# Kernel optimization log

Hardware: AMD Instinct MI355X
Metric: run time of the kernel (lower is better)

Reference implementation:

```python
import jax, jax.numpy as jnp
import numpy as np


def setup_inputs() -> dict:
    key = jax.random.key(0)
    k1, k2, k3, k4 = jax.random.split(key, 4)
    B, Nq, Nk, D = 8, 2048, 2048, 768
    return {
        "query": jax.random.normal(k1, (B, Nq, D), dtype=jnp.float32),
        "key": jax.random.normal(k2, (Nk, D), dtype=jnp.float32),
        "x": jax.random.normal(k3, (B, Nk, D), dtype=jnp.float32),
        "W": jax.random.normal(k4, (D, D), dtype=jnp.float32) * (1.0 / np.sqrt(D)),
        "b": jnp.zeros((D,), dtype=jnp.float32),
    }


def reference(query, key, x, W, b):
    # Linear projection: [B,Nq,dk] @ W^T + b -> [B,Nq,dq]
    query_proj = jnp.einsum("bqd,ed->bqe", query, W) + b
    # tensordot over dim_query: [B,Nq,dq] x [Nk,dq] -> [B,Nq,Nk]
    score = jnp.einsum("bqe,ke->bqk", query_proj, key)
    attn = jax.nn.softmax(score, axis=-1)
    # bmm: [B,Nq,Nk] @ [B,Nk,Dv] -> [B,Nq,Dv]
    out = jnp.einsum("bqk,bkd->bqd", attn, x)
    return (out, attn)
```

## Files before the change

kernel.cpp:

```cpp
#include <hip/hip_runtime.h>

typedef short s16x8 __attribute__((ext_vector_type(8)));
typedef _Float16 h16x8 __attribute__((ext_vector_type(8)));
typedef float f32x4 __attribute__((ext_vector_type(4)));

__device__ __forceinline__ unsigned short f2bf(float f) {
    unsigned int u = __builtin_bit_cast(unsigned int, f);
    u += 0x7FFFu + ((u >> 16) & 1u);
    return (unsigned short)(u >> 16);
}
__device__ __forceinline__ float bf2f(unsigned short h) {
    unsigned int u = ((unsigned int)h) << 16;
    return __builtin_bit_cast(float, u);
}
__device__ __forceinline__ unsigned short f2h(float f) {
    _Float16 h = (_Float16)f;
    return __builtin_bit_cast(unsigned short, h);
}
__device__ __forceinline__ float h2f(unsigned short u) {
    return (float)__builtin_bit_cast(_Float16, u);
}

__device__ __forceinline__ int swz(int row, int kbyte) {
    return (row * 64 + kbyte) ^ (((row >> 1) & 3) << 4);
}

__device__ __forceinline__ void gl16(const void* g, void* l) {
    __builtin_amdgcn_global_load_lds(
        (__attribute__((address_space(1))) void*)(g),
        (__attribute__((address_space(3))) void*)(l), 16, 0, 0);
}

#define STG(ptr, rowbase, tau, bufp, slot) do {                                     \
    gl16((ptr) + (long)((rowbase) + sl) * K + (tau) * 64 + koff,                    \
         &lds[bufp][slot][(unsigned)t * 8]);                                        \
    gl16((ptr) + (long)((rowbase) + 64 + sl) * K + (tau) * 64 + koff,               \
         &lds[bufp][slot][4096u + (unsigned)t * 8]);                                \
} while (0)

#define PH(bufp, qi, qj, VMSTR, STAGEBLOCK) do {                                    \
    h16x8 af_[2][4], bf_[2][2];                                                     \
    const char* baseA_ = (const char*)&lds[bufp][qi][0];                            \
    const char* baseB_ = (const char*)&lds[bufp][2 + (qj)][0];                      \
    _Pragma("unroll")                                                               \
    for (int ks_ = 0; ks_ < 2; ++ks_) {                                             \
        _Pragma("unroll")                                                           \
        for (int f_ = 0; f_ < 4; ++f_) {                                            \
            const int row_ = wm * 64 + f_ * 16 + lr;                                \
            af_[ks_][f_] = *(const h16x8*)(baseA_ + row_ * 128 +                    \
                            ((ks_ * 64 + kg16) ^ ((row_ & 7) << 4)));               \
        }                                                                           \
        _Pragma("unroll")                                                           \
        for (int g_ = 0; g_ < 2; ++g_) {                                            \
            const int row_ = wn * 32 + g_ * 16 + lr;                                \
            bf_[ks_][g_] = *(const h16x8*)(baseB_ + row_ * 128 +                    \
                            ((ks_ * 64 + kg16) ^ ((row_ & 7) << 4)));               \
        }                                                                           \
    }                                                                               \
    STAGEBLOCK;                                                                     \
    asm volatile("s_waitcnt vmcnt(" VMSTR ")" ::: "memory");                        \
    __builtin_amdgcn_s_barrier();                                                   \
    __builtin_amdgcn_sched_barrier(0);                                              \
    __builtin_amdgcn_s_setprio(1);                                                  \
    _Pragma("unroll")                                                               \
    for (int ks_ = 0; ks_ < 2; ++ks_)                                               \
        _Pragma("unroll")                                                           \
        for (int f_ = 0; f_ < 4; ++f_)                                              \
            _Pragma("unroll")                                                       \
            for (int g_ = 0; g_ < 2; ++g_)                                          \
                acc[qi][qj][f_][g_] = __builtin_amdgcn_mfma_f32_16x16x32_f16(       \
                    af_[ks_][f_], bf_[ks_][g_], acc[qi][qj][f_][g_], 0, 0, 0);      \
    __builtin_amdgcn_s_setprio(0);                                                  \
    __builtin_amdgcn_s_barrier();                                                   \
    __builtin_amdgcn_sched_barrier(0);                                              \
} while (0)

__global__ __launch_bounds__(512, 2) void score_8ph(
    const unsigned short* __restrict__ A, const unsigned short* __restrict__ Bm,
    const float* __restrict__ bias, float* __restrict__ C,
    int M, int N, int K, int nbx)
{
    __shared__ unsigned short lds[2][4][8192];

    const int bid = blockIdx.x;
    const int cpx = gridDim.x >> 3;
    const int sw  = (bid & 7) * cpx + (bid >> 3);
    const int m0 = (sw / nbx) * 256, n0 = (sw % nbx) * 256;

    const int t = threadIdx.x;
    const int l = t & 63, w = t >> 6;
    const int wm = w >> 2, wn = w & 3;
    const int lr = l & 15;
    const int kg16 = (l >> 4) * 16;

    const int sl   = w * 8 + (l >> 3);
    const int koff = ((l & 7) ^ (sl & 7)) * 8;

    f32x4 acc[2][2][4][2];
    #pragma unroll
    for (int a = 0; a < 2; ++a)
        #pragma unroll
        for (int b = 0; b < 2; ++b)
            #pragma unroll
            for (int c = 0; c < 4; ++c)
                #pragma unroll
                for (int d = 0; d < 2; ++d)
                    acc[a][b][c][d] = (f32x4){0.f, 0.f, 0.f, 0.f};

    const int nt = K >> 6;

    STG(A,  m0,       0, 0, 0);
    STG(Bm, n0,       0, 0, 2);
    STG(A,  m0 + 128, 0, 0, 1);
    STG(Bm, n0 + 128, 0, 0, 3);
    STG(A,  m0,       1, 1, 0);
    STG(Bm, n0,       1, 1, 2);
    asm volatile("s_waitcnt vmcnt(8)" ::: "memory");
    __builtin_amdgcn_s_barrier();
    __builtin_amdgcn_sched_barrier(0);

    int tau = 0;
    for (; tau < nt - 2; ++tau) {
        const int bp = tau & 1;
        PH(bp, 0, 0, "6",  { STG(A,  m0 + 128, tau + 1, bp ^ 1, 1); });
        PH(bp, 0, 1, "10", { STG(Bm, n0 + 128, tau + 1, bp ^ 1, 3); });
        PH(bp, 1, 0, "10", { STG(A,  m0,       tau + 2, bp,     0); });
        PH(bp, 1, 1, "8",  { STG(Bm, n0,       tau + 2, bp,     2); });
    }
    {
        const int bp = tau & 1;
        PH(bp, 0, 0, "6",  { STG(A,  m0 + 128, tau + 1, bp ^ 1, 1); });
        PH(bp, 0, 1, "10", { STG(Bm, n0 + 128, tau + 1, bp ^ 1, 3); });
        PH(bp, 1, 0, "10", {});
        PH(bp, 1, 1, "8",  {});
        ++tau;
    }
    {
        const int bp = tau & 1;
        PH(bp, 0, 0, "0", {});
        PH(bp, 0, 1, "0", {});
        PH(bp, 1, 0, "0", {});
        PH(bp, 1, 1, "0", {});
    }

    #pragma unroll
    for (int qi = 0; qi < 2; ++qi)
        #pragma unroll
        for (int qj = 0; qj < 2; ++qj)
            #pragma unroll
            for (int f = 0; f < 4; ++f)
                #pragma unroll
                for (int g = 0; g < 2; ++g) {
                    const int row = m0 + qi * 128 + wm * 64 + f * 16 + (l >> 4) * 4;
                    const int col = n0 + qj * 128 + wn * 32 + g * 16 + lr;
                    const float badd = bias[col];
                    #pragma unroll
                    for (int r = 0; r < 4; ++r)
                        C[(long)(row + r) * N + col] = acc[qi][qj][f][g][r] + badd;
                }
}

__global__ __launch_bounds__(256, 1) void pv_2ph(
    const unsigned short* __restrict__ A, const unsigned short* __restrict__ Bm,
    float* __restrict__ C, int M, int N, int K,
    long strideA, long strideB, long strideC)
{
    __shared__ unsigned short lds[2][2][128 * 64];

    const int bz = blockIdx.z;
    const unsigned short* Ab = A  + (long)bz * strideA;
    const unsigned short* Bb = Bm + (long)bz * strideB;
    float* Cb = C + (long)bz * strideC;
    const int m0 = blockIdx.x * 128, n0 = blockIdx.y * 128;

    const int t = threadIdx.x;
    const int l = t & 63, w = t >> 6;
    const int rm = (w >> 1) * 64, cn = (w & 1) * 64;
    const int lr = l & 15;
    const int kg16 = (l >> 4) * 16;

    const int jrow   = l >> 3;
    const int srcoff = ((l & 7) ^ jrow) << 3;

    const unsigned short* gA = Ab + (long)(m0 + jrow) * K + srcoff;
    const unsigned short* gB = Bb + (long)(n0 + jrow) * K + srcoff;

    f32x4 acc[4][4];
    #pragma unroll
    for (int i = 0; i < 4; ++i)
        #pragma unroll
        for (int j = 0; j < 4; ++j)
            acc[i][j] = (f32x4){0.f, 0.f, 0.f, 0.f};

    const int nt = K >> 6;
    #pragma unroll
    for (int i = 0; i < 4; ++i) {
        const int c = w * 4 + i;
        gl16(gA + (long)(8 * c) * K, &lds[0][0][c * 512]);
        gl16(gB + (long)(8 * c) * K, &lds[0][1][c * 512]);
    }
    __syncthreads();

    int p = 0;
    for (int it = 0; it < nt; ++it) {
        if (it + 1 < nt) {
            const unsigned short* nA = gA + (it + 1) * 64;
            const unsigned short* nB = gB + (it + 1) * 64;
            #pragma unroll
            for (int i = 0; i < 4; ++i) {
                const int c = w * 4 + i;
                gl16(nA + (long)(8 * c) * K, &lds[p ^ 1][0][c * 512]);
                gl16(nB + (long)(8 * c) * K, &lds[p ^ 1][1][c * 512]);
            }
        }
        const char* baseA = (const char*)&lds[p][0][0];
        const char* baseB = (const char*)&lds[p][1][0];
        h16x8 af[2][4], bf[2][4];
        #pragma unroll
        for (int ks = 0; ks < 2; ++ks)
            #pragma unroll
            for (int mi = 0; mi < 4; ++mi) {
                const int row = rm + mi * 16 + lr;
                af[ks][mi] = *(const h16x8*)(baseA + row * 128 +
                                ((ks * 64 + kg16) ^ ((row & 7) << 4)));
            }
        #pragma unroll
        for (int ks = 0; ks < 2; ++ks)
            #pragma unroll
            for (int nj = 0; nj < 4; ++nj) {
                const int row = cn + nj * 16 + lr;
                bf[ks][nj] = *(const h16x8*)(baseB + row * 128 +
                                ((ks * 64 + kg16) ^ ((row & 7) << 4)));
            }
        #pragma unroll
        for (int ks = 0; ks < 2; ++ks)
            #pragma unroll
            for (int mi = 0; mi < 4; ++mi)
                #pragma unroll
                for (int nj = 0; nj < 4; ++nj)
                    acc[mi][nj] = __builtin_amdgcn_mfma_f32_16x16x32_f16(
                        af[ks][mi], bf[ks][nj], acc[mi][nj], 0, 0, 0);
        __syncthreads();
        p ^= 1;
    }

    #pragma unroll
    for (int mi = 0; mi < 4; ++mi) {
        #pragma unroll
        for (int nj = 0; nj < 4; ++nj) {
            const int row = m0 + rm + mi * 16 + (l >> 4) * 4;
            const int col = n0 + cn + nj * 16 + lr;
            #pragma unroll
            for (int r = 0; r < 4; ++r)
                Cb[(long)(row + r) * N + col] = acc[mi][nj][r];
        }
    }
}

template<int SPLIT, bool TRANSB, bool BIAS>
__global__ __launch_bounds__(256, 1) void mfma_gemm(
    const float* __restrict__ A, const float* __restrict__ Bsrc,
    const float* __restrict__ bias, float* __restrict__ C,
    int M, int N, int K, long strideA, long strideB, long strideC)
{
    constexpr int NB = (SPLIT > 1) ? 2 : 1;
    __shared__ unsigned short sA[NB][128 * 32];
    __shared__ unsigned short sB[NB][128 * 32];

    const int t  = threadIdx.x;
    const int bz = blockIdx.z;
    const float* Ab = A    + (long)bz * strideA;
    const float* Bb = Bsrc + (long)bz * strideB;
    float*       Cb = C    + (long)bz * strideC;
    const int m0 = blockIdx.y * 128;
    const int n0 = blockIdx.x * 128;

    const int l  = t & 63, w = t >> 6;
    const int rm = (w >> 1) * 64;
    const int cn = (w & 1) * 64;
    const int lr = l & 15;
    const int kg = (l >> 4) * 16;

    const int srow = t >> 1;
    const int skh  = (t & 1) * 16;
    const int s_ = t & 15;
    const int kp = t >> 4;

    f32x4 acc[4][4];
    #pragma unroll
    for (int i = 0; i < 4; ++i)
        #pragma unroll
        for (int j = 0; j < 4; ++j)
            acc[i][j] = (f32x4){0.f, 0.f, 0.f, 0.f};

    for (int kt = 0; kt < K; kt += 32) {
        {
            const float* p = &Ab[(long)(m0 + srow) * K + kt + skh];
            float f[16];
            #pragma unroll
            for (int q = 0; q < 4; ++q) {
                const float4 v = *(const float4*)(p + 4 * q);
                f[4*q+0] = v.x; f[4*q+1] = v.y; f[4*q+2] = v.z; f[4*q+3] = v.w;
            }
            s16x8 h0, h1, l0, l1;
            #pragma unroll
            for (int q = 0; q < 8; ++q) {
                unsigned short h = f2bf(f[q]);      h0[q] = (short)h;
                if (SPLIT > 1) l0[q] = (short)f2bf(f[q] - bf2f(h));
                unsigned short g = f2bf(f[8 + q]);  h1[q] = (short)g;
                if (SPLIT > 1) l1[q] = (short)f2bf(f[8 + q] - bf2f(g));
            }
            *(s16x8*)((char*)sA[0] + swz(srow, skh * 2))      = h0;
            *(s16x8*)((char*)sA[0] + swz(srow, skh * 2 + 16)) = h1;
            if (SPLIT > 1) {
                *(s16x8*)((char*)sA[1] + swz(srow, skh * 2))      = l0;
                *(s16x8*)((char*)sA[1] + swz(srow, skh * 2 + 16)) = l1;
            }
        }
        if (!TRANSB) {
            const float* p = &Bb[(long)(n0 + srow) * K + kt + skh];
            float f[16];
            #pragma unroll
            for (int q = 0; q < 4; ++q) {
                const float4 v = *(const float4*)(p + 4 * q);
                f[4*q+0] = v.x; f[4*q+1] = v.y; f[4*q+2] = v.z; f[4*q+3] = v.w;
            }
            s16x8 h0, h1, l0, l1;
            #pragma unroll
            for (int q = 0; q < 8; ++q) {
                unsigned short h = f2bf(f[q]);      h0[q] = (short)h;
                if (SPLIT > 1) l0[q] = (short)f2bf(f[q] - bf2f(h));
                unsigned short g = f2bf(f[8 + q]);  h1[q] = (short)g;
                if (SPLIT > 1) l1[q] = (short)f2bf(f[8 + q] - bf2f(g));
            }
            *(s16x8*)((char*)sB[0] + swz(srow, skh * 2))      = h0;
            *(s16x8*)((char*)sB[0] + swz(srow, skh * 2 + 16)) = h1;
            if (SPLIT > 1) {
                *(s16x8*)((char*)sB[1] + swz(srow, skh * 2))      = l0;
                *(s16x8*)((char*)sB[1] + swz(srow, skh * 2 + 16)) = l1;
            }
        } else {
            const float* r0 = &Bb[(long)(kt + 2 * kp) * N + n0 + s_ * 8];
            const float* r1 = r0 + N;
            float a0[8], a1[8];
            {
                const float4 u0 = *(const float4*)(r0);
                const float4 u1 = *(const float4*)(r0 + 4);
                const float4 v0 = *(const float4*)(r1);
                const float4 v1 = *(const float4*)(r1 + 4);
                a0[0]=u0.x;a0[1]=u0.y;a0[2]=u0.z;a0[3]=u0.w;
                a0[4]=u1.x;a0[5]=u1.y;a0[6]=u1.z;a0[7]=u1.w;
                a1[0]=v0.x;a1[1]=v0.y;a1[2]=v0.z;a1[3]=v0.w;
                a1[4]=v1.x;a1[5]=v1.y;a1[6]=v1.z;a1[7]=v1.w;
            }
            #pragma unroll
            for (int j = 0; j < 8; ++j) {
                const int i  = (j + s_) & 7;
                const int nl = s_ * 8 + i;
                const unsigned int val =
                    (unsigned int)f2bf(a0[i]) | ((unsigned int)f2bf(a1[i]) << 16);
                *(unsigned int*)((char*)sB[0] + swz(nl, 4 * kp)) = val;
            }
        }
        __syncthreads();

        s16x8 ah[4], bh[4];
        #pragma unroll
        for (int mi = 0; mi < 4; ++mi)
            ah[mi] = *(const s16x8*)((const char*)sA[0] + swz(rm + mi * 16 + lr, kg));
        #pragma unroll
        for (int nj = 0; nj < 4; ++nj)
            bh[nj] = *(const s16x8*)((const char*)sB[0] + swz(cn + nj * 16 + lr, kg));
        #pragma unroll
        for (int mi = 0; mi < 4; ++mi)
            #pragma unroll
            for (int nj = 0; nj < 4; ++nj)
                acc[mi][nj] = __builtin_amdgcn_mfma_f32_16x16x32_bf16(
                    ah[mi], bh[nj], acc[mi][nj], 0, 0, 0);
        if (SPLIT > 1) {
            s16x8 al[4], bl[4];
            #pragma unroll
            for (int mi = 0; mi < 4; ++mi)
                al[mi] = *(const s16x8*)((const char*)sA[1] + swz(rm + mi * 16 + lr, kg));
            #pragma unroll
            for (int mi = 0; mi < 4; ++mi)
                #pragma unroll
                for (int nj = 0; nj < 4; ++nj)
                    acc[mi][nj] = __builtin_amdgcn_mfma_f32_16x16x32_bf16(
                        al[mi], bh[nj], acc[mi][nj], 0, 0, 0);
            #pragma unroll
            for (int nj = 0; nj < 4; ++nj)
                bl[nj] = *(const s16x8*)((const char*)sB[1] + swz(cn + nj * 16 + lr, kg));
            #pragma unroll
            for (int mi = 0; mi < 4; ++mi)
                #pragma unroll
                for (int nj = 0; nj < 4; ++nj)
                    acc[mi][nj] = __builtin_amdgcn_mfma_f32_16x16x32_bf16(
                        ah[mi], bl[nj], acc[mi][nj], 0, 0, 0);
        }
        __syncthreads();
    }

    #pragma unroll
    for (int mi = 0; mi < 4; ++mi) {
        #pragma unroll
        for (int nj = 0; nj < 4; ++nj) {
            const int row = m0 + rm + mi * 16 + (l >> 4) * 4;
            const int col = n0 + cn + nj * 16 + lr;
            const float badd = BIAS ? bias[col] : 0.f;
            #pragma unroll
            for (int r = 0; r < 4; ++r)
                Cb[(long)(row + r) * N + col] = acc[mi][nj][r] + badd;
        }
    }
}

__global__ __launch_bounds__(256, 1) void score_gemm(
    const unsigned short* __restrict__ Ah, const unsigned short* __restrict__ Al,
    const unsigned short* __restrict__ Bh, const unsigned short* __restrict__ Bl,
    const float* __restrict__ bias, float* __restrict__ C,
    int M, int N, int K, int nbx)
{
    __shared__ unsigned short sAh[128 * 32];
    __shared__ unsigned short sBh[128 * 32];
    __shared__ unsigned short sAl[128 * 32];
    __shared__ unsigned short sBl[128 * 32];

    const int bid = blockIdx.x;
    const int cpx = gridDim.x >> 3;
    const int sw  = (bid & 7) * cpx + (bid >> 3);
    const int mb  = sw / nbx, nb = sw % nbx;
    const int m0 = mb * 128, n0 = nb * 128;

    const int t = threadIdx.x;
    const int l = t & 63, w = t >> 6;
    const int rm = (w >> 1) * 64;
    const int cn = (w & 1) * 64;
    const int lr = l & 15;
    const int kg = (l >> 4) * 16;

    const int r0 = 2 * w, r1 = 2 * w + 1;
    const int rowS0 = 16 * r0 + (l >> 2);
    const int rowS1 = 16 * r1 + (l >> 2);
    const int h0 = (l & 3) ^ ((rowS0 >> 1) & 3);
    const int h1 = (l & 3) ^ ((rowS1 >> 1) & 3);

    const unsigned short* gAh0 = Ah + (long)(m0 + rowS0) * K + 8 * h0;
    const unsigned short* gAh1 = Ah + (long)(m0 + rowS1) * K + 8 * h1;
    const unsigned short* gAl0 = Al + (long)(m0 + rowS0) * K + 8 * h0;
    const unsigned short* gAl1 = Al + (long)(m0 + rowS1) * K + 8 * h1;
    const unsigned short* gBh0 = Bh + (long)(n0 + rowS0) * K + 8 * h0;
    const unsigned short* gBh1 = Bh + (long)(n0 + rowS1) * K + 8 * h1;
    const unsigned short* gBl0 = Bl + (long)(n0 + rowS0) * K + 8 * h0;
    const unsigned short* gBl1 = Bl + (long)(n0 + rowS1) * K + 8 * h1;

    unsigned short* dA0 = &sAh[r0 * 512];
    unsigned short* dA1 = &sAh[r1 * 512];
    unsigned short* dAl0 = &sAl[r0 * 512];
    unsigned short* dAl1 = &sAl[r1 * 512];
    unsigned short* dB0 = &sBh[r0 * 512];
    unsigned short* dB1 = &sBh[r1 * 512];
    unsigned short* dBl0 = &sBl[r0 * 512];
    unsigned short* dBl1 = &sBl[r1 * 512];

    f32x4 acc[4][4];
    #pragma unroll
    for (int i = 0; i < 4; ++i)
        #pragma unroll
        for (int j = 0; j < 4; ++j)
            acc[i][j] = (f32x4){0.f, 0.f, 0.f, 0.f};

    const int nk = K >> 5;
    for (int it = 0; it < nk; ++it) {
        gl16(gAh0, dA0);  gl16(gAh1, dA1);
        gl16(gBh0, dB0);  gl16(gBh1, dB1);
        gl16(gAl0, dAl0); gl16(gAl1, dAl1);
        gl16(gBl0, dBl0); gl16(gBl1, dBl1);
        gAh0 += 32; gAh1 += 32; gAl0 += 32; gAl1 += 32;
        gBh0 += 32; gBh1 += 32; gBl0 += 32; gBl1 += 32;
        __syncthreads();

        s16x8 ah[4], bh[4];
        #pragma unroll
        for (int mi = 0; mi < 4; ++mi)
            ah[mi] = *(const s16x8*)((const char*)sAh + swz(rm + mi * 16 + lr, kg));
        #pragma unroll
        for (int nj = 0; nj < 4; ++nj)
            bh[nj] = *(const s16x8*)((const char*)sBh + swz(cn + nj * 16 + lr, kg));
        #pragma unroll
        for (int mi = 0; mi < 4; ++mi)
            #pragma unroll
            for (int nj = 0; nj < 4; ++nj)
                acc[mi][nj] = __builtin_amdgcn_mfma_f32_16x16x32_bf16(
                    ah[mi], bh[nj], acc[mi][nj], 0, 0, 0);
        s16x8 al[4], bl[4];
        #pragma unroll
        for (int mi = 0; mi < 4; ++mi)
            al[mi] = *(const s16x8*)((const char*)sAl + swz(rm + mi * 16 + lr, kg));
        #pragma unroll
        for (int mi = 0; mi < 4; ++mi)
            #pragma unroll
            for (int nj = 0; nj < 4; ++nj)
                acc[mi][nj] = __builtin_amdgcn_mfma_f32_16x16x32_bf16(
                    al[mi], bh[nj], acc[mi][nj], 0, 0, 0);
        #pragma unroll
        for (int nj = 0; nj < 4; ++nj)
            bl[nj] = *(const s16x8*)((const char*)sBl + swz(cn + nj * 16 + lr, kg));
        #pragma unroll
        for (int mi = 0; mi < 4; ++mi)
            #pragma unroll
            for (int nj = 0; nj < 4; ++nj)
                acc[mi][nj] = __builtin_amdgcn_mfma_f32_16x16x32_bf16(
                    ah[mi], bl[nj], acc[mi][nj], 0, 0, 0);
        __syncthreads();
    }

    #pragma unroll
    for (int mi = 0; mi < 4; ++mi) {
        #pragma unroll
        for (int nj = 0; nj < 4; ++nj) {
            const int row = m0 + rm + mi * 16 + (l >> 4) * 4;
            const int col = n0 + cn + nj * 16 + lr;
            const float badd = bias[col];
            #pragma unroll
            for (int r = 0; r < 4; ++r)
                C[(long)(row + r) * N + col] = acc[mi][nj][r] + badd;
        }
    }
}

__global__ __launch_bounds__(256, 1) void out_gemm(
    const float* __restrict__ A32, const unsigned short* __restrict__ B16,
    float* __restrict__ C, int M, int N, int K,
    long strideA, long strideB, long strideC)
{
    __shared__ unsigned short sA[128 * 32];
    __shared__ unsigned short sB[128 * 32];

    const int bz = blockIdx.z;
    const float* Ab = A32 + (long)bz * strideA;
    const unsigned short* Bb = B16 + (long)bz * strideB;
    float* Cb = C + (long)bz * strideC;
    const int m0 = blockIdx.x * 128;
    const int n0 = blockIdx.y * 128;

    const int t = threadIdx.x;
    const int l = t & 63, w = t >> 6;
    const int rm = (w >> 1) * 64;
    const int cn = (w & 1) * 64;
    const int lr = l & 15;
    const int kg = (l >> 4) * 16;

    const int r0 = 2 * w, r1 = 2 * w + 1;
    const int rowS0 = 16 * r0 + (l >> 2);
    const int rowS1 = 16 * r1 + (l >> 2);
    const int h0 = (l & 3) ^ ((rowS0 >> 1) & 3);
    const int h1 = (l & 3) ^ ((rowS1 >> 1) & 3);
    const unsigned short* gB0 = Bb + (long)(n0 + rowS0) * K + 8 * h0;
    const unsigned short* gB1 = Bb + (long)(n0 + rowS1) * K + 8 * h1;
    unsigned short* dB0 = &sB[r0 * 512];
    unsigned short* dB1 = &sB[r1 * 512];

    const int srow = t >> 1;
    const int skh  = (t & 1) * 16;
    const float* gA = &Ab[(long)(m0 + srow) * K + skh];

    f32x4 acc[4][4];
    #pragma unroll
    for (int i = 0; i < 4; ++i)
        #pragma unroll
        for (int j = 0; j < 4; ++j)
            acc[i][j] = (f32x4){0.f, 0.f, 0.f, 0.f};

    const int nk = K >> 5;
    for (int it = 0; it < nk; ++it) {
        gl16(gB0, dB0); gl16(gB1, dB1);
        gB0 += 32; gB1 += 32;
        {
            float f[16];
            #pragma unroll
            for (int q = 0; q < 4; ++q) {
                const float4 v = *(const float4*)(gA + 4 * q);
                f[4*q+0] = v.x; f[4*q+1] = v.y; f[4*q+2] = v.z; f[4*q+3] = v.w;
            }
            gA += 32;
            s16x8 v0, v1;
            #pragma unroll
            for (int q = 0; q < 8; ++q) {
                v0[q] = (short)f2bf(f[q]);
                v1[q] = (short)f2bf(f[8 + q]);
            }
            *(s16x8*)((char*)sA + swz(srow, skh * 2))      = v0;
            *(s16x8*)((char*)sA + swz(srow, skh * 2 + 16)) = v1;
        }
        __syncthreads();

        s16x8 ah[4], bh[4];
        #pragma unroll
        for (int mi = 0; mi < 4; ++mi)
            ah[mi] = *(const s16x8*)((const char*)sA + swz(rm + mi * 16 + lr, kg));
        #pragma unroll
        for (int nj = 0; nj < 4; ++nj)
            bh[nj] = *(const s16x8*)((const char*)sB + swz(cn + nj * 16 + lr, kg));
        #pragma unroll
        for (int mi = 0; mi < 4; ++mi)
            #pragma unroll
            for (int nj = 0; nj < 4; ++nj)
                acc[mi][nj] = __builtin_amdgcn_mfma_f32_16x16x32_bf16(
                    ah[mi], bh[nj], acc[mi][nj], 0, 0, 0);
        __syncthreads();
    }

    #pragma unroll
    for (int mi = 0; mi < 4; ++mi) {
        #pragma unroll
        for (int nj = 0; nj < 4; ++nj) {
            const int row = m0 + rm + mi * 16 + (l >> 4) * 4;
            const int col = n0 + cn + nj * 16 + lr;
            #pragma unroll
            for (int r = 0; r < 4; ++r)
                Cb[(long)(row + r) * N + col] = acc[mi][nj][r];
        }
    }
}

template<int MODE>
__global__ __launch_bounds__(256) void transpose64(
    const float* __restrict__ in, void* __restrict__ outv,
    int R, int Cc, long sIn, long sOut)
{
    __shared__ float tl[64][65];
    const int z = blockIdx.z;
    const float* ib = in + (long)z * sIn;
    const int r0 = blockIdx.x * 64, c0 = blockIdx.y * 64;
    const int t = threadIdx.x;
    const int lrr = t >> 4, lc = (t & 15) * 4;
    #pragma unroll
    for (int p = 0; p < 4; ++p) {
        const float4 v = *(const float4*)&ib[(long)(r0 + lrr + 16 * p) * Cc + c0 + lc];
        tl[lrr + 16 * p][lc + 0] = v.x; tl[lrr + 16 * p][lc + 1] = v.y;
        tl[lrr + 16 * p][lc + 2] = v.z; tl[lrr + 16 * p][lc + 3] = v.w;
    }
    __syncthreads();
    #pragma unroll
    for (int p = 0; p < 4; ++p) {
        const int orow = c0 + lrr + 16 * p;
        const int ocol = r0 + lc;
        const float a = tl[lc + 0][lrr + 16 * p];
        const float b = tl[lc + 1][lrr + 16 * p];
        const float c = tl[lc + 2][lrr + 16 * p];
        const float d = tl[lc + 3][lrr + 16 * p];
        if (MODE == 1) {
            ushort4 u = { f2bf(a), f2bf(b), f2bf(c), f2bf(d) };
            *(ushort4*)((unsigned short*)outv + (long)z * sOut + (long)orow * R + ocol) = u;
        } else if (MODE == 2) {
            ushort4 u = { f2h(a), f2h(b), f2h(c), f2h(d) };
            *(ushort4*)((unsigned short*)outv + (long)z * sOut + (long)orow * R + ocol) = u;
        } else {
            float4 u = { a, b, c, d };
            *(float4*)((float*)outv + (long)z * sOut + (long)orow * R + ocol) = u;
        }
    }
}

__global__ __launch_bounds__(256) void convert_hilo(
    const float* __restrict__ src, unsigned short* __restrict__ hi,
    unsigned short* __restrict__ lo, long n8)
{
    for (long i = (long)blockIdx.x * blockDim.x + threadIdx.x; i < n8;
         i += (long)gridDim.x * blockDim.x) {
        const float4 a = *(const float4*)&src[i * 8];
        const float4 b = *(const float4*)&src[i * 8 + 4];
        const float f[8] = { a.x, a.y, a.z, a.w, b.x, b.y, b.z, b.w };
        s16x8 h, lv;
        #pragma unroll
        for (int q = 0; q < 8; ++q) {
            const unsigned short hh = f2bf(f[q]);
            h[q]  = (short)hh;
            lv[q] = (short)f2bf(f[q] - bf2f(hh));
        }
        *(s16x8*)&hi[i * 8] = h;
        *(s16x8*)&lo[i * 8] = lv;
    }
}

__global__ __launch_bounds__(256) void convert_q_ilv(
    const float* __restrict__ src, unsigned short* __restrict__ dst,
    int kd8, long n8)
{
    const int Kd = kd8 * 8;
    for (long i = (long)blockIdx.x * blockDim.x + threadIdx.x; i < n8;
         i += (long)gridDim.x * blockDim.x) {
        const long row = i / kd8;
        const int  col = (int)(i - row * kd8) * 8;
        const float4 a = *(const float4*)&src[i * 8];
        const float4 b = *(const float4*)&src[i * 8 + 4];
        const float f[8] = { a.x, a.y, a.z, a.w, b.x, b.y, b.z, b.w };
        s16x8 h, lv;
        #pragma unroll
        for (int q = 0; q < 8; ++q) {
            const unsigned short hh = f2h(f[q]);
            h[q]  = (short)hh;
            lv[q] = (short)f2h(f[q] - h2f(hh));
        }
        unsigned short* dr = dst + row * (long)(2 * Kd);
        *(s16x8*)&dr[col]      = h;
        *(s16x8*)&dr[Kd + col] = lv;
    }
}

__global__ __launch_bounds__(256) void convert_kw_dup(
    const float* __restrict__ src, unsigned short* __restrict__ dst,
    int kd8, long n8)
{
    const int Kd = kd8 * 8;
    for (long i = (long)blockIdx.x * blockDim.x + threadIdx.x; i < n8;
         i += (long)gridDim.x * blockDim.x) {
        const long row = i / kd8;
        const int  col = (int)(i - row * kd8) * 8;
        const float4 a = *(const float4*)&src[i * 8];
        const float4 b = *(const float4*)&src[i * 8 + 4];
        const float f[8] = { a.x, a.y, a.z, a.w, b.x, b.y, b.z, b.w };
        s16x8 h;
        #pragma unroll
        for (int q = 0; q < 8; ++q) h[q] = (short)f2h(f[q]);
        unsigned short* dr = dst + row * (long)(2 * Kd);
        *(s16x8*)&dr[col]      = h;
        *(s16x8*)&dr[Kd + col] = h;
    }
}

__global__ __launch_bounds__(256) void bk_dot(
    const float* __restrict__ key, const float* __restrict__ b,
    float* __restrict__ bk, int D)
{
    const int row = blockIdx.x * 4 + (threadIdx.x >> 6);
    const int l = threadIdx.x & 63;
    const float* kr = key + (long)row * D;
    float s = 0.f;
    for (int e = l; e < D; e += 64) s += kr[e] * b[e];
    #pragma unroll
    for (int off = 32; off > 0; off >>= 1) s += __shfl_xor(s, off);
    if (l == 0) bk[row] = s;
}

__global__ __launch_bounds__(256) void softmax_f16(
    float* __restrict__ S, unsigned short* __restrict__ S16, int cols)
{
    const long row = blockIdx.x;
    float* p = S + row * (long)cols;
    unsigned short* p16 = S16 + row * (long)cols;
    const int t = threadIdx.x;
    const int wid = t >> 6;
    const int base = t * 8;

    const float4 a = *(const float4*)&p[base];
    const float4 b = *(const float4*)&p[base + 4];
    float vals[8] = { a.x, a.y, a.z, a.w, b.x, b.y, b.z, b.w };
    float m = -INFINITY;
    #pragma unroll
    for (int i = 0; i < 8; ++i) m = fmaxf(m, vals[i]);
    #pragma unroll
    for (int off = 32; off > 0; off >>= 1)
        m = fmaxf(m, __shfl_xor(m, off));
    __shared__ float smax[4], ssum[4];
    if ((t & 63) == 0) smax[wid] = m;
    __syncthreads();
    m = fmaxf(fmaxf(smax[0], smax[1]), fmaxf(smax[2], smax[3]));

    float s = 0.f;
    #pragma unroll
    for (int i = 0; i < 8; ++i) {
        vals[i] = __expf(vals[i] - m);
        s += vals[i];
    }
    #pragma unroll
    for (int off = 32; off > 0; off >>= 1)
        s += __shfl_xor(s, off);
    if ((t & 63) == 0) ssum[wid] = s;
    __syncthreads();
    s = (ssum[0] + ssum[1]) + (ssum[2] + ssum[3]);
    const float inv = 1.0f / s;

    float4 o0, o1;
    o0.x = vals[0]*inv; o0.y = vals[1]*inv; o0.z = vals[2]*inv; o0.w = vals[3]*inv;
    o1.x = vals[4]*inv; o1.y = vals[5]*inv; o1.z = vals[6]*inv; o1.w = vals[7]*inv;
    *(float4*)&p[base]     = o0;
    *(float4*)&p[base + 4] = o1;
    s16x8 h;
    h[0]=(short)f2h(o0.x); h[1]=(short)f2h(o0.y); h[2]=(short)f2h(o0.z); h[3]=(short)f2h(o0.w);
    h[4]=(short)f2h(o1.x); h[5]=(short)f2h(o1.y); h[6]=(short)f2h(o1.z); h[7]=(short)f2h(o1.w);
    *(s16x8*)&p16[base] = h;
}

__global__ __launch_bounds__(256) void softmax_rows(float* __restrict__ S, int cols)
{
    const long row = blockIdx.x;
    float* p = S + row * (long)cols;
    const int t = threadIdx.x;
    const int wid = t >> 6;

    float vals[8];
    float m = -INFINITY;
    #pragma unroll
    for (int i = 0; i < 8; ++i) {
        vals[i] = p[t + i * 256];
        m = fmaxf(m, vals[i]);
    }
    #pragma unroll
    for (int off = 32; off > 0; off >>= 1)
        m = fmaxf(m, __shfl_xor(m, off));
    __shared__ float smax[4], ssum[4];
    if ((t & 63) == 0) smax[wid] = m;
    __syncthreads();
    m = fmaxf(fmaxf(smax[0], smax[1]), fmaxf(smax[2], smax[3]));

    float s = 0.f;
    #pragma unroll
    for (int i = 0; i < 8; ++i) {
        vals[i] = __expf(vals[i] - m);
        s += vals[i];
    }
    #pragma unroll
    for (int off = 32; off > 0; off >>= 1)
        s += __shfl_xor(s, off);
    if ((t & 63) == 0) ssum[wid] = s;
    __syncthreads();
    s = (ssum[0] + ssum[1]) + (ssum[2] + ssum[3]);
    const float inv = 1.0f / s;
    #pragma unroll
    for (int i = 0; i < 8; ++i)
        p[t + i * 256] = vals[i] * inv;
}

extern "C" void kernel_launch(void* const* d_in, const int* in_sizes, int n_in,
                              void* d_out, int out_size, void* d_ws, size_t ws_size,
                              hipStream_t stream)
{
    const float* query = (const float*)d_in[0];
    const float* key   = (const float*)d_in[1];
    const float* x     = (const float*)d_in[2];
    const float* W     = (const float*)d_in[3];
    const float* bias  = (const float*)d_in[4];

    const int D  = in_sizes[4];
    const int Nk = in_sizes[1] / D;
    const int B  = in_sizes[2] / (Nk * D);
    const int Nq = in_sizes[0] / (B * D);

    float* out  = (float*)d_out;
    float* attn = out + (long)B * Nq * D;

    const long nQ  = (long)B * Nq * D;
    const long nKW = (long)Nk * D;
    const long nX  = (long)B * Nk * D;
    const int  M   = B * Nq;
    const int  K2  = 2 * D;

    const size_t xTb    = (size_t)nX * 2;
    const size_t kwDupB = (size_t)Nk * K2 * 2;
    const size_t bkB    = (size_t)Nk * 4;
    const size_t atb1   = (size_t)Nq * Nk * 2;
    const size_t fixedB = xTb + kwDupB + bkB;
    const size_t qLob   = (size_t)nQ * 2;
    const size_t wsMid  = xTb + qLob;

    int g = 0;
    if (ws_size >= fixedB + 2 * atb1) {
        g = (int)((ws_size - fixedB) / atb1);
        if (g > B) g = B;
    }

    if (g >= 2) {
        unsigned short* qIlv  = (unsigned short*)out;
        unsigned short* xT     = (unsigned short*)d_ws;
        unsigned short* kwDup  = (unsigned short*)((char*)d_ws + xTb);
        float*          bk     = (float*)((char*)d_ws + xTb + kwDupB);
        unsigned short* attn16 = (unsigned short*)((char*)d_ws + fixedB);
        float* Wt  = attn;
        float* KWf = attn + 1048576;

        dim3 gtw(D / 64, D / 64, 1);
        transpose64<0><<<gtw, 256, 0, stream>>>(W, Wt, D, D, 0L, 0L);
        dim3 gkw(D / 128, Nk / 128, 1);
        mfma_gemm<3, false, false><<<gkw, 256, 0, stream>>>(
            key, Wt, nullptr, KWf, Nk, D, D, 0L, 0L, 0L);
        convert_kw_dup<<<768, 256, 0, stream>>>(KWf, kwDup, D / 8, nKW / 8);
        bk_dot<<<Nk / 4, 256, 0, stream>>>(key, bias, bk, D);
        convert_q_ilv<<<2048, 256, 0, stream>>>(query, qIlv, D / 8, nQ / 8);
        dim3 gtx(Nk / 64, D / 64, B);
        transpose64<2><<<gtx, 256, 0, stream>>>(
            x, xT, Nk, D, (long)Nk * D, (long)D * Nk);

        const int nbx = Nk / 256;
        const int nwg = (M / 256) * nbx;
        score_8ph<<<nwg, 512, 0, stream>>>(
            qIlv, kwDup, bk, attn, M, Nk, K2, nbx);

        for (int b0 = 0; b0 < B; b0 += g) {
            const int gb = (b0 + g <= B) ? g : (B - b0);
            softmax_f16<<<gb * Nq, 256, 0, stream>>>(
                attn + (long)b0 * Nq * Nk, attn16, Nk);
            dim3 go(Nq / 128, D / 128, gb);
            pv_2ph<<<go, 256, 0, stream>>>(
                attn16, xT + (long)b0 * D * Nk, out + (long)b0 * Nq * D,
                Nq, D, Nk, (long)Nq * Nk, (long)D * Nk, (long)Nq * D);
        }
    } else if (ws_size >= wsMid) {
        unsigned short* q_hi  = (unsigned short*)out;
        unsigned short* KW_hi = q_hi + nQ;
        unsigned short* KW_lo = KW_hi + nKW;
        float*          bk    = (float*)(KW_lo + nKW);
        unsigned short* q_lo  = (unsigned short*)d_ws;
        unsigned short* xT    = q_lo + nQ;
        float* Wt  = attn;
        float* KWf = attn + 1048576;

        dim3 gtw(D / 64, D / 64, 1);
        transpose64<0><<<gtw, 256, 0, stream>>>(W, Wt, D, D, 0L, 0L);
        dim3 gkw(D / 128, Nk / 128, 1);
        mfma_gemm<3, false, false><<<gkw, 256, 0, stream>>>(
            key, Wt, nullptr, KWf, Nk, D, D, 0L, 0L, 0L);
        convert_hilo<<<768, 256, 0, stream>>>(KWf, KW_hi, KW_lo, nKW / 8);
        bk_dot<<<Nk / 4, 256, 0, stream>>>(key, bias, bk, D);
        convert_hilo<<<2048, 256, 0, stream>>>(query, q_hi, q_lo, nQ / 8);
        dim3 gtx(Nk / 64, D / 64, B);
        transpose64<1><<<gtx, 256, 0, stream>>>(
            x, xT, Nk, D, (long)Nk * D, (long)D * Nk);
        const int nbx = Nk / 128;
        const int nwg = (B * Nq / 128) * nbx;
        score_gemm<<<nwg, 256, 0, stream>>>(
            q_hi, q_lo, KW_hi, KW_lo, bk, attn, B * Nq, Nk, D, nbx);
        softmax_rows<<<B * Nq, 256, 0, stream>>>(attn, Nk);
        dim3 go(Nq / 128, D / 128, B);
        out_gemm<<<go, 256, 0, stream>>>(
            attn, xT, out, Nq, D, Nk, (long)Nq * Nk, (long)D * Nk, (long)Nq * D);
    } else {
        float* qp = out;
        dim3 g1(D / 128, (B * Nq) / 128, 1);
        mfma_gemm<3, false, true><<<g1, 256, 0, stream>>>(
            query, W, bias, qp, B * Nq, D, D, 0L, 0L, 0L);
        dim3 g2(Nk / 128, Nq / 128, B);
        mfma_gemm<3, false, false><<<g2, 256, 0, stream>>>(
            qp, key, nullptr, attn, Nq, Nk, D, (long)Nq * D, 0L, (long)Nq * Nk);
        softmax_rows<<<B * Nq, 256, 0, stream>>>(attn, Nk);
        dim3 g4(D / 128, Nq / 128, B);
        mfma_gemm<1, true, false><<<g4, 256, 0, stream>>>(
            attn, x, nullptr, out, Nq, D, Nk, (long)Nq * Nk, (long)Nk * D, (long)Nq * D);
    }
}
```

Measured before the change: 348.8 us.

## Reuse LDS fragments across quadrant phases with serpentine MFMA ordering

Restructures the 8-wave score GEMM main loop so A and B fragments read from LDS are kept in registers and reused across quadrant phases. The new order is (0,0),(0,1),(1,1),(1,0), and staging order and vmcnt thresholds are reworked to match. This cuts LDS reads per K-tile from four A+B fragment sets to two A and two B. In exchange it holds more fragment registers live, which may pressure occupancy at the 512x2 launch bound, and the changed wait counts must stay correct.

```diff
diff --git a/kernel.cpp b/kernel.cpp
--- a/kernel.cpp
+++ b/kernel.cpp
@@ -31,36 +31,44 @@
         (__attribute__((address_space(3))) void*)(l), 16, 0, 0);
 }
 
-#define STG(ptr, rowbase, tau, bufp, slot) do {                                     \
-    gl16((ptr) + (long)((rowbase) + sl) * K + (tau) * 64 + koff,                    \
+#define STG(ptr, rowbase, tt, bufp, slot) do {                                      \
+    gl16((ptr) + (long)((rowbase) + sl) * K + (tt) * 64 + koff,                     \
          &lds[bufp][slot][(unsigned)t * 8]);                                        \
-    gl16((ptr) + (long)((rowbase) + 64 + sl) * K + (tau) * 64 + koff,               \
+    gl16((ptr) + (long)((rowbase) + 64 + sl) * K + (tt) * 64 + koff,                \
          &lds[bufp][slot][4096u + (unsigned)t * 8]);                                \
 } while (0)
 
-#define PH(bufp, qi, qj, VMSTR, STAGEBLOCK) do {                                    \
-    h16x8 af_[2][4], bf_[2][2];                                                     \
-    const char* baseA_ = (const char*)&lds[bufp][qi][0];                            \
-    const char* baseB_ = (const char*)&lds[bufp][2 + (qj)][0];                      \
+#define LDA(qi_) do {                                                               \
+    const char* ba_ = (const char*)&lds[bp][qi_][0];                                \
     _Pragma("unroll")                                                               \
-    for (int ks_ = 0; ks_ < 2; ++ks_) {                                             \
+    for (int ks_ = 0; ks_ < 2; ++ks_)                                               \
         _Pragma("unroll")                                                           \
         for (int f_ = 0; f_ < 4; ++f_) {                                            \
             const int row_ = wm * 64 + f_ * 16 + lr;                                \
-            af_[ks_][f_] = *(const h16x8*)(baseA_ + row_ * 128 +                    \
+            af[ks_][f_] = *(const h16x8*)(ba_ + row_ * 128 +                        \
                             ((ks_ * 64 + kg16) ^ ((row_ & 7) << 4)));               \
         }                                                                           \
+} while (0)
+
+#define LDB(dst_, qj_) do {                                                         \
+    const char* bb_ = (const char*)&lds[bp][2 + (qj_)][0];                          \
+    _Pragma("unroll")                                                               \
+    for (int ks_ = 0; ks_ < 2; ++ks_)                                               \
         _Pragma("unroll")                                                           \
         for (int g_ = 0; g_ < 2; ++g_) {                                            \
             const int row_ = wn * 32 + g_ * 16 + lr;                                \
-            bf_[ks_][g_] = *(const h16x8*)(baseB_ + row_ * 128 +                    \
+            dst_[ks_][g_] = *(const h16x8*)(bb_ + row_ * 128 +                      \
                             ((ks_ * 64 + kg16) ^ ((row_ & 7) << 4)));               \
         }                                                                           \
-    }                                                                               \
-    STAGEBLOCK;                                                                     \
+} while (0)
+
+#define SYNCV(VMSTR) do {                                                           \
     asm volatile("s_waitcnt vmcnt(" VMSTR ")" ::: "memory");                        \
     __builtin_amdgcn_s_barrier();                                                   \
     __builtin_amdgcn_sched_barrier(0);                                              \
+} while (0)
+
+#define MM(qi_, qj_, bfv_) do {                                                     \
     __builtin_amdgcn_s_setprio(1);                                                  \
     _Pragma("unroll")                                                               \
     for (int ks_ = 0; ks_ < 2; ++ks_)                                               \
@@ -68,8 +76,8 @@
         for (int f_ = 0; f_ < 4; ++f_)                                              \
             _Pragma("unroll")                                                       \
             for (int g_ = 0; g_ < 2; ++g_)                                          \
-                acc[qi][qj][f_][g_] = __builtin_amdgcn_mfma_f32_16x16x32_f16(       \
-                    af_[ks_][f_], bf_[ks_][g_], acc[qi][qj][f_][g_], 0, 0, 0);      \
+                acc[qi_][qj_][f_][g_] = __builtin_amdgcn_mfma_f32_16x16x32_f16(     \
+                    af[ks_][f_], bfv_[ks_][g_], acc[qi_][qj_][f_][g_], 0, 0, 0);    \
     __builtin_amdgcn_s_setprio(0);                                                  \
     __builtin_amdgcn_s_barrier();                                                   \
     __builtin_amdgcn_sched_barrier(0);                                              \
@@ -96,6 +104,7 @@
     const int sl   = w * 8 + (l >> 3);
     const int koff = ((l & 7) ^ (sl & 7)) * 8;
 
+    h16x8 af[2][4], bf0[2][2], bf1[2][2];
     f32x4 acc[2][2][4][2];
     #pragma unroll
     for (int a = 0; a < 2; ++a)
@@ -111,8 +120,8 @@
 
     STG(A,  m0,       0, 0, 0);
     STG(Bm, n0,       0, 0, 2);
+    STG(Bm, n0 + 128, 0, 0, 3);
     STG(A,  m0 + 128, 0, 0, 1);
-    STG(Bm, n0 + 128, 0, 0, 3);
     STG(A,  m0,       1, 1, 0);
     STG(Bm, n0,       1, 1, 2);
     asm volatile("s_waitcnt vmcnt(8)" ::: "memory");
@@ -122,25 +131,52 @@
     int tau = 0;
     for (; tau < nt - 2; ++tau) {
         const int bp = tau & 1;
-        PH(bp, 0, 0, "6",  { STG(A,  m0 + 128, tau + 1, bp ^ 1, 1); });
-        PH(bp, 0, 1, "10", { STG(Bm, n0 + 128, tau + 1, bp ^ 1, 3); });
-        PH(bp, 1, 0, "10", { STG(A,  m0,       tau + 2, bp,     0); });
-        PH(bp, 1, 1, "8",  { STG(Bm, n0,       tau + 2, bp,     2); });
+        LDA(0); LDB(bf0, 0);
+        STG(Bm, n0 + 128, tau + 1, bp ^ 1, 3);
+        SYNCV("8");
+        MM(0, 0, bf0);
+        LDB(bf1, 1);
+        STG(A, m0 + 128, tau + 1, bp ^ 1, 1);
+        SYNCV("8");
+        MM(0, 1, bf1);
+        LDA(1);
+        STG(A, m0, tau + 2, bp, 0);
+        SYNCV("10");
+        MM(1, 1, bf1);
+        STG(Bm, n0, tau + 2, bp, 2);
+        SYNCV("8");
+        MM(1, 0, bf0);
     }
     {
         const int bp = tau & 1;
-        PH(bp, 0, 0, "6",  { STG(A,  m0 + 128, tau + 1, bp ^ 1, 1); });
-        PH(bp, 0, 1, "10", { STG(Bm, n0 + 128, tau + 1, bp ^ 1, 3); });
-        PH(bp, 1, 0, "10", {});
-        PH(bp, 1, 1, "8",  {});
+        LDA(0); LDB(bf0, 0);
+        STG(Bm, n0 + 128, tau + 1, bp ^ 1, 3);
+        SYNCV("8");
+        MM(0, 0, bf0);
+        LDB(bf1, 1);
+        STG(A, m0 + 128, tau + 1, bp ^ 1, 1);
+        SYNCV("8");
+        MM(0, 1, bf1);
+        LDA(1);
+        SYNCV("8");
+        MM(1, 1, bf1);
+        SYNCV("4");
+        MM(1, 0, bf0);
         ++tau;
     }
     {
         const int bp = tau & 1;
-        PH(bp, 0, 0, "0", {});
-        PH(bp, 0, 1, "0", {});
-        PH(bp, 1, 0, "0", {});
-        PH(bp, 1, 1, "0", {});
+        LDA(0); LDB(bf0, 0);
+        SYNCV("2");
+        MM(0, 0, bf0);
+        LDB(bf1, 1);
+        SYNCV("0");
+        MM(0, 1, bf1);
+        LDA(1);
+        SYNCV("0");
+        MM(1, 1, bf1);
+        SYNCV("0");
+        MM(1, 0, bf0);
     }
 
     #pragma unroll
```

New measurement: 336.8 us. 3.4% less time.
